# Optimization experiments

Hardware: AMD Instinct MI355X
Metric: run time of the kernel (lower is better)

The kernel has to match this reference:

```python
import jax, jax.numpy as jnp
import numpy as np

B, L, D, N = 2, 2048, 1024, 16
DT = 0.1  # liquid scaler integration step


def setup_inputs() -> dict:
    key = jax.random.key(0)
    ks = jax.random.split(key, 10)
    def w(k, shape, scale=0.02):
        return jax.random.normal(k, shape, jnp.float32) * scale
    log_min, log_max = float(np.log(0.001)), float(np.log(0.1))
    dt_bias = jax.random.uniform(ks[1], (D,), jnp.float32) * (log_max - log_min) + log_min
    return {
        "x": jax.random.normal(ks[0], (B, L, D), jnp.float32),
        "delta_W": w(ks[2], (D, D)), "delta_b": jnp.zeros((D,), jnp.float32),
        "B_W": w(ks[3], (N, D)), "B_b": jnp.zeros((N,), jnp.float32),
        "C_W": w(ks[4], (N, D)), "C_b": jnp.zeros((N,), jnp.float32),
        "A_log": jnp.zeros((D, N), jnp.float32),
        "dt_bias": dt_bias,
        "tau": jnp.ones((N,), jnp.float32),
        "Wi_W": w(ks[5], (N, D)), "Wi_b": jnp.zeros((N,), jnp.float32),
        "Wr_W": w(ks[6], (N, N)),
        "sel_W": w(ks[7], (D, N)), "sel_b": jnp.zeros((D,), jnp.float32),
        "h0": jnp.zeros((1, N), jnp.float32),
    }


def reference(x, delta_W, delta_b, B_W, B_b, C_W, C_b, A_log, dt_bias, tau,
              Wi_W, Wi_b, Wr_W, sel_W, sel_b, h0):
    Bsz, Ls, Dm = x.shape
    Ns = A_log.shape[1]

    # --- LiquidTimeConstantScaler ---
    gc = x.mean(axis=1)                                # [B, D]
    inp_sig = gc @ Wi_W.T + Wi_b                       # [B, N]
    cur = jnp.broadcast_to(h0, (Bsz, Ns))              # [B, N]
    rec = cur @ Wr_W.T                                 # [B, N]
    tau_c = jnp.clip(tau, 0.1, 10.0)
    dh_dt = (-cur + jnp.tanh(inp_sig + rec)) / tau_c[None, :]
    new_h = cur + DT * dh_dt                           # [B, N]
    sel = jax.nn.sigmoid(new_h @ sel_W.T + sel_b)      # [B, D]
    xs = x * sel[:, None, :]                           # [B, L, D]

    # --- selective SSM discretization ---
    delta = jax.nn.softplus(xs @ delta_W.T + delta_b + dt_bias)  # [B, L, D]
    Bm = xs @ B_W.T + B_b                              # [B, L, N]
    Cm = xs @ C_W.T + C_b                              # [B, L, N]
    A = -jnp.exp(A_log)                                # [D, N]
    A_d = jnp.exp(A[None, None] * delta[..., None])    # [B, L, D, N]
    factor = jnp.where(jnp.abs(A)[None, None] < 1e-6,
                       delta[..., None], (A_d - 1.0) / A[None, None])
    B_d = factor * Bm[:, :, None, :]                   # [B, L, D, N]

    # --- linear recurrence over time via scan ---
    def step(h, inputs):
        Ad_t, Bd_t, x_t, C_t = inputs                  # [B,D,N],[B,D,N],[B,D],[B,N]
        h = Ad_t * h + Bd_t * x_t[..., None]
        y = jnp.einsum('bdn,bn->bd', h, C_t)
        return h, y

    h_init = jnp.zeros((Bsz, Dm, Ns), x.dtype)
    _, ys = jax.lax.scan(step, h_init,
                         (A_d.transpose(1, 0, 2, 3), B_d.transpose(1, 0, 2, 3),
                          xs.transpose(1, 0, 2), Cm.transpose(1, 0, 2)))
    return ys.transpose(1, 0, 2)                        # [B, L, D]
```

## Files before the change

kernel.cpp:

```cpp
#include <hip/hip_runtime.h>
#include <hip/hip_bf16.h>
#include <math.h>

#define B_ 2
#define L_ 2048
#define D_ 1024
#define N_ 16
#define CCH 64
#define TCH 32
#define NCOLS 1056
#define NPAD  1088

typedef unsigned short u16;
typedef __attribute__((ext_vector_type(8))) short short8v;
typedef __attribute__((ext_vector_type(8))) unsigned short ushort8v;
typedef __attribute__((ext_vector_type(4))) float f32x4;

__device__ __forceinline__ float softplusf(float z) {
  return fmaxf(z, 0.f) + log1pf(__expf(-fabsf(z)));
}

__device__ __forceinline__ u16 bf16rne(float f) {
  union { float f; unsigned u; } c; c.f = f;
  unsigned u = c.u;
  u += 0x7fffu + ((u >> 16) & 1u);
  return (u16)(u >> 16);
}

__device__ __forceinline__ float bf16tof(u16 v) {
  union { unsigned u; float f; } c;
  c.u = (unsigned)v << 16;
  return c.f;
}

__device__ __forceinline__ void gl_lds16(const void* g, const u16* lds_base,
                                         int byte_off) {
  byte_off = __builtin_amdgcn_readfirstlane(byte_off);
  __builtin_amdgcn_global_load_lds(
      (const __attribute__((address_space(1))) void*)g,
      (__attribute__((address_space(3))) void*)((const char*)lds_base + byte_off),
      16, 0, 0);
}

__global__ __launch_bounds__(256) void k_gc_pack(const float* __restrict__ x,
    float* __restrict__ part1, u16* __restrict__ xb) {
  int blk = blockIdx.x;
  int b = blk >> 8, lc = blk & 255;
  int tid = threadIdx.x;
  int r0 = b * L_ + lc * 8;
  float4 s = {0.f, 0.f, 0.f, 0.f};
  #pragma unroll
  for (int q = 0; q < 8; ++q) {
    size_t off = (size_t)(r0 + q) * D_ + tid * 4;
    float4 v = *(const float4*)(x + off);
    s.x += v.x; s.y += v.y; s.z += v.z; s.w += v.w;
    ushort4 r;
    r.x = bf16rne(v.x); r.y = bf16rne(v.y);
    r.z = bf16rne(v.z); r.w = bf16rne(v.w);
    *(ushort4*)(xb + off) = r;
  }
  *(float4*)(part1 + (size_t)blk * D_ + tid * 4) = s;
}

__global__ __launch_bounds__(256) void k_gc_red(const float* __restrict__ part1,
                                                float* __restrict__ part2) {
  int gid = blockIdx.x * 256 + threadIdx.x;
  int d = gid & 1023;
  int jc = (gid >> 10) & 15;
  int b = gid >> 14;
  float s = 0.f;
  #pragma unroll
  for (int t = 0; t < 16; ++t)
    s += part1[(size_t)(b * 256 + jc * 16 + t) * D_ + d];
  part2[gid] = s;
}

__global__ __launch_bounds__(256) void k_newh_sel(const float* __restrict__ part2,
    const float* __restrict__ Wi_W, const float* __restrict__ Wi_b,
    const float* __restrict__ Wr_W, const float* __restrict__ tau,
    const float* __restrict__ h0, const float* __restrict__ sel_W,
    const float* __restrict__ sel_b, float* __restrict__ selp) {
  __shared__ float gcs[B_ * D_];
  __shared__ float nh[B_ * N_];
  int tid = threadIdx.x;
  for (int idx = tid; idx < B_ * D_; idx += 256) {
    int b = idx >> 10, d = idx & (D_ - 1);
    float s = 0.f;
    #pragma unroll
    for (int lc = 0; lc < 16; ++lc)
      s += part2[(size_t)((b << 4) | lc) * D_ + d];
    gcs[idx] = s * (1.f / L_);
  }
  __syncthreads();
  if (tid < B_ * N_) {
    int b = tid >> 4, n = tid & 15;
    float inp = Wi_b[n];
    const float* g = gcs + b * D_;
    const float* w = Wi_W + n * D_;
    for (int d = 0; d < D_; d += 4) {
      float4 gv = *(const float4*)(g + d);
      float4 wv = *(const float4*)(w + d);
      inp += gv.x * wv.x + gv.y * wv.y + gv.z * wv.z + gv.w * wv.w;
    }
    float rec = 0.f;
    for (int m = 0; m < N_; ++m) rec += h0[m] * Wr_W[n * N_ + m];
    float th = tanhf(inp + rec);
    float tc = fminf(fmaxf(tau[n], 0.1f), 10.f);
    float cur = h0[n];
    nh[tid] = cur + 0.1f * ((th - cur) / tc);
  }
  __syncthreads();
  for (int i = tid; i < B_ * D_; i += 256) {
    int b = i >> 10, d = i & (D_ - 1);
    const float* w = sel_W + d * N_;
    const float* h = nh + b * N_;
    float z = sel_b[d];
    #pragma unroll
    for (int n = 0; n < N_; n += 4) {
      float4 wv = *(const float4*)(w + n);
      z += h[n] * wv.x + h[n + 1] * wv.y + h[n + 2] * wv.z + h[n + 3] * wv.w;
    }
    selp[i] = 1.f / (1.f + __expf(-z));
  }
}

__global__ __launch_bounds__(256) void k_pack_w(const float* __restrict__ dW,
    const float* __restrict__ B_W, const float* __restrict__ C_W,
    const float* __restrict__ sel, u16* __restrict__ Wp) {
  int gid = blockIdx.x * 256 + threadIdx.x;
  int b = blockIdx.y;
  size_t e = (size_t)gid * 8;
  int nn = (int)(e >> 10);
  int k = (int)(e & 1023);
  ushort8v r;
  if (nn < NCOLS) {
    const float* src = (nn < 1024) ? dW + (size_t)nn * 1024
                     : (nn < 1040) ? B_W + (size_t)(nn - 1024) * 1024
                                   : C_W + (size_t)(nn - 1040) * 1024;
    float4 s0 = *(const float4*)(src + k);
    float4 s1 = *(const float4*)(src + k + 4);
    const float* sp = sel + b * D_ + k;
    float4 e0 = *(const float4*)sp;
    float4 e1 = *(const float4*)(sp + 4);
    r[0] = bf16rne(s0.x * e0.x); r[1] = bf16rne(s0.y * e0.y);
    r[2] = bf16rne(s0.z * e0.z); r[3] = bf16rne(s0.w * e0.w);
    r[4] = bf16rne(s1.x * e1.x); r[5] = bf16rne(s1.y * e1.y);
    r[6] = bf16rne(s1.z * e1.z); r[7] = bf16rne(s1.w * e1.w);
  } else {
    r = (ushort8v)0;
  }
  *(ushort8v*)(Wp + (size_t)b * (NPAD * 1024) + e) = r;
}

__global__ __launch_bounds__(256) void k_gemm(
    const u16* __restrict__ xb, const u16* __restrict__ Wp,
    const float* __restrict__ delta_b, const float* __restrict__ dt_bias,
    const float* __restrict__ B_b, const float* __restrict__ C_b,
    float* __restrict__ delta, float* __restrict__ Bm, float* __restrict__ Cm) {
  __shared__ __align__(16) u16 lds[4][4096];
  int m0 = blockIdx.x * 64;
  int n0 = blockIdx.y * 64;
  int batch = blockIdx.x >> 5;
  const u16* wb = Wp + (size_t)batch * (NPAD * 1024);
  int tid = threadIdx.x;
  int w = tid >> 6, l = tid & 63;
  int wr = w >> 1, wc = w & 1;
  int srow = l >> 3;
  int ssl = (l & 7) ^ srow;

  f32x4 acc[2][2];
  #pragma unroll
  for (int m = 0; m < 2; ++m)
    #pragma unroll
    for (int n = 0; n < 2; ++n)
      acc[m][n] = (f32x4){0.f, 0.f, 0.f, 0.f};

  #define STAGE(kb, buf)                                                       \
    {                                                                          \
      _Pragma("unroll")                                                        \
      for (int q = 0; q < 2; ++q) {                                            \
        int row = w * 16 + q * 8 + srow;                                       \
        gl_lds16(xb + (size_t)(m0 + row) * 1024 + (kb) * 64 + ssl * 8,         \
                 &lds[0][0], (buf) * 8192 + (w * 16 + q * 8) * 128);           \
        gl_lds16(wb + (size_t)(n0 + row) * 1024 + (kb) * 64 + ssl * 8,         \
                 &lds[0][0], 16384 + (buf) * 8192 + (w * 16 + q * 8) * 128);   \
      }                                                                        \
    }

  int lr = l & 15, lh = l >> 4;

  #define CSTEP(cur)                                                           \
    {                                                                          \
      _Pragma("unroll")                                                        \
      for (int ks = 0; ks < 2; ++ks) {                                         \
        short8v a[2], bq[2];                                                   \
        _Pragma("unroll")                                                      \
        for (int m = 0; m < 2; ++m) {                                          \
          int r = wr * 32 + m * 16 + lr;                                       \
          int ps = (ks * 4 + lh) ^ (r & 7);                                    \
          a[m] = *(const short8v*)((const char*)&lds[0][0] + (cur) * 8192 + r * 128 + ps * 16);\
        }                                                                      \
        _Pragma("unroll")                                                      \
        for (int n = 0; n < 2; ++n) {                                          \
          int r = wc * 32 + n * 16 + lr;                                       \
          int ps = (ks * 4 + lh) ^ (r & 7);                                    \
          bq[n] = *(const short8v*)((const char*)&lds[0][0] + 16384 + (cur) * 8192 + r * 128 + ps * 16);\
        }                                                                      \
        _Pragma("unroll")                                                      \
        for (int m = 0; m < 2; ++m)                                            \
          _Pragma("unroll")                                                    \
          for (int n = 0; n < 2; ++n)                                          \
            acc[m][n] = __builtin_amdgcn_mfma_f32_16x16x32_bf16(a[m], bq[n],   \
                                                                acc[m][n], 0, 0, 0);\
      }                                                                        \
    }

  STAGE(0, 0);
  STAGE(1, 1);
  #pragma unroll
  for (int kb = 0; kb < 15; ++kb) {
    int cur = kb & 1;
    asm volatile("s_waitcnt vmcnt(4)" ::: "memory");
    __builtin_amdgcn_s_barrier();
    CSTEP(cur);
    asm volatile("s_waitcnt lgkmcnt(0)" ::: "memory");
    __builtin_amdgcn_s_barrier();
    if (kb < 14) STAGE(kb + 2, cur);
  }
  asm volatile("s_waitcnt vmcnt(0)" ::: "memory");
  __builtin_amdgcn_s_barrier();
  CSTEP(1);
  #undef STAGE
  #undef CSTEP

  int ibase = m0 + wr * 32 + lh * 4;
  int jbase = n0 + wc * 32 + lr;
  #pragma unroll
  for (int m = 0; m < 2; ++m) {
    #pragma unroll
    for (int n = 0; n < 2; ++n) {
      int j = jbase + n * 16;
      #pragma unroll
      for (int r = 0; r < 2 * 2; ++r) {
        int i = ibase + m * 16 + r;
        float v = acc[m][n][r];
        if (j < 1024) {
          delta[(size_t)i * D_ + j] = softplusf(v + delta_b[j] + dt_bias[j]);
        } else if (j < 1040) {
          Bm[i * N_ + (j - 1024)] = v + B_b[j - 1024];
        } else if (j < NCOLS) {
          Cm[i * N_ + (j - 1040)] = v + C_b[j - 1040];
        }
      }
    }
  }
}

__global__ __launch_bounds__(256) void k_scan1(const u16* __restrict__ xb,
    const float* __restrict__ sel, const float* __restrict__ delta,
    const float* __restrict__ Bm, const float* __restrict__ A_log,
    float* __restrict__ prodA, float* __restrict__ hend) {
  int gid = blockIdx.x * 256 + threadIdx.x;
  int nq = gid & 3;
  int d = (gid >> 2) & (D_ - 1);
  int c = (gid >> 12) & (CCH - 1);
  int b = gid >> 18;
  float A[4], rA[4];
  unsigned smallm = 0;
  {
    float4 a0 = *(const float4*)(A_log + d * N_ + nq * 4);
    float av[4] = {a0.x, a0.y, a0.z, a0.w};
    #pragma unroll
    for (int n = 0; n < 4; ++n) {
      float a = -__expf(av[n]);
      A[n] = a; rA[n] = 1.f / a;
      if (fabsf(a) < 1e-6f) smallm |= (1u << n);
    }
  }
  float selv = sel[b * D_ + d];
  float h[4], p[4];
  #pragma unroll
  for (int n = 0; n < 4; ++n) { h[n] = 0.f; p[n] = 1.f; }
  int row0 = b * L_ + c * TCH;
  const u16* xp = xb + (size_t)row0 * D_ + d;
  const float* dp = delta + (size_t)row0 * D_ + d;
  const float4* bmp = (const float4*)(Bm + (size_t)row0 * N_) + nq;
  #pragma unroll 4
  for (int s = 0; s < TCH; ++s) {
    float dlt = dp[(size_t)s * D_];
    float xv = bf16tof(xp[(size_t)s * D_]) * selv;
    float4 q0 = bmp[s * 4];
    float bmv[4] = {q0.x, q0.y, q0.z, q0.w};
    #pragma unroll
    for (int n = 0; n < 4; ++n) {
      float Ad = __expf(A[n] * dlt);
      float f = ((smallm >> n) & 1u) ? dlt : (Ad - 1.f) * rA[n];
      h[n] = Ad * h[n] + (f * bmv[n]) * xv;
      p[n] *= Ad;
    }
  }
  size_t base = ((size_t)(gid >> 2)) * N_ + nq * 4;
  *(float4*)(prodA + base) = make_float4(p[0], p[1], p[2], p[3]);
  *(float4*)(hend + base)  = make_float4(h[0], h[1], h[2], h[3]);
}

__global__ __launch_bounds__(256) void k_scan2(const float* __restrict__ prodA,
    const float* __restrict__ hend, float* __restrict__ hin) {
  int gid = blockIdx.x * 256 + threadIdx.x;
  int b = gid >> 14;
  int rem = gid & 16383;
  size_t base = ((size_t)(b * CCH) << 14) + rem;
  float H = 0.f;
  #pragma unroll
  for (int g = 0; g < 4; ++g) {
    float pg[16], hg[16];
    #pragma unroll
    for (int t = 0; t < 16; ++t) {
      size_t idx = base + ((size_t)(g * 16 + t) << 14);
      pg[t] = prodA[idx];
      hg[t] = hend[idx];
    }
    #pragma unroll
    for (int t = 0; t < 16; ++t) {
      size_t idx = base + ((size_t)(g * 16 + t) << 14);
      hin[idx] = H;
      H = pg[t] * H + hg[t];
    }
  }
}

__global__ __launch_bounds__(256) void k_scan3(const u16* __restrict__ xb,
    const float* __restrict__ sel, const float* __restrict__ delta,
    const float* __restrict__ Bm, const float* __restrict__ Cm,
    const float* __restrict__ A_log, const float* __restrict__ hin,
    float* __restrict__ out) {
  int gid = blockIdx.x * 256 + threadIdx.x;
  int nq = gid & 3;
  int d = (gid >> 2) & (D_ - 1);
  int c = (gid >> 12) & (CCH - 1);
  int b = gid >> 18;
  float A[4], rA[4];
  unsigned smallm = 0;
  {
    float4 a0 = *(const float4*)(A_log + d * N_ + nq * 4);
    float av[4] = {a0.x, a0.y, a0.z, a0.w};
    #pragma unroll
    for (int n = 0; n < 4; ++n) {
      float a = -__expf(av[n]);
      A[n] = a; rA[n] = 1.f / a;
      if (fabsf(a) < 1e-6f) smallm |= (1u << n);
    }
  }
  float selv = sel[b * D_ + d];
  float h[4];
  {
    size_t base = ((size_t)(gid >> 2)) * N_ + nq * 4;
    float4 v0 = *(const float4*)(hin + base);
    h[0] = v0.x; h[1] = v0.y; h[2] = v0.z; h[3] = v0.w;
  }
  int row0 = b * L_ + c * TCH;
  const u16* xp = xb + (size_t)row0 * D_ + d;
  const float* dp = delta + (size_t)row0 * D_ + d;
  const float4* bmp = (const float4*)(Bm + (size_t)row0 * N_) + nq;
  const float4* cmp = (const float4*)(Cm + (size_t)row0 * N_) + nq;
  float* op = out + (size_t)row0 * D_ + d;
  #pragma unroll 4
  for (int s = 0; s < TCH; ++s) {
    float dlt = dp[(size_t)s * D_];
    float xv = bf16tof(xp[(size_t)s * D_]) * selv;
    float4 q0 = bmp[s * 4];
    float4 r0 = cmp[s * 4];
    float bmv[4] = {q0.x, q0.y, q0.z, q0.w};
    float cmv[4] = {r0.x, r0.y, r0.z, r0.w};
    float yp = 0.f;
    #pragma unroll
    for (int n = 0; n < 4; ++n) {
      float Ad = __expf(A[n] * dlt);
      float f = ((smallm >> n) & 1u) ? dlt : (Ad - 1.f) * rA[n];
      h[n] = Ad * h[n] + (f * bmv[n]) * xv;
      yp += h[n] * cmv[n];
    }
    float y = yp + __shfl_xor(yp, 1, 64);
    y += __shfl_xor(y, 2, 64);
    if (nq == 0) op[(size_t)s * D_] = y;
  }
}

extern "C" void kernel_launch(void* const* d_in, const int* in_sizes, int n_in,
                              void* d_out, int out_size, void* d_ws, size_t ws_size,
                              hipStream_t stream) {
  const float* x       = (const float*)d_in[0];
  const float* deltaW  = (const float*)d_in[1];
  const float* deltab  = (const float*)d_in[2];
  const float* B_W     = (const float*)d_in[3];
  const float* B_b     = (const float*)d_in[4];
  const float* C_W     = (const float*)d_in[5];
  const float* C_b     = (const float*)d_in[6];
  const float* A_log   = (const float*)d_in[7];
  const float* dt_bias = (const float*)d_in[8];
  const float* tau     = (const float*)d_in[9];
  const float* Wi_W    = (const float*)d_in[10];
  const float* Wi_b    = (const float*)d_in[11];
  const float* Wr_W    = (const float*)d_in[12];
  const float* sel_W   = (const float*)d_in[13];
  const float* sel_b   = (const float*)d_in[14];
  const float* h0      = (const float*)d_in[15];
  float* out = (float*)d_out;

  float* ws    = (float*)d_ws;
  float* delta = ws;
  float* selp  = delta + 4194304;
  float* Bm    = selp + 2048;
  float* Cm    = Bm + 65536;
  u16*   xb    = (u16*)(Cm + 65536);
  u16*   Wp    = xb + 4194304;
  float* hin   = (float*)(Wp + 2228224);
  float* part1 = hin;
  float* part2 = hin + 524288;
  float* prodA = out;
  float* hend  = out + 2097152;

  hipLaunchKernelGGL(k_gc_pack, dim3(512), dim3(256), 0, stream, x, part1, xb);
  hipLaunchKernelGGL(k_gc_red, dim3(128), dim3(256), 0, stream, part1, part2);
  hipLaunchKernelGGL(k_newh_sel, dim3(1), dim3(256), 0, stream,
                     part2, Wi_W, Wi_b, Wr_W, tau, h0, sel_W, sel_b, selp);
  hipLaunchKernelGGL(k_pack_w, dim3(544, 2), dim3(256), 0, stream,
                     deltaW, B_W, C_W, selp, Wp);
  hipLaunchKernelGGL(k_gemm, dim3(64, 17), dim3(256), 0, stream,
                     xb, Wp, deltab, dt_bias, B_b, C_b, delta, Bm, Cm);
  hipLaunchKernelGGL(k_scan1, dim3(2048), dim3(256), 0, stream,
                     xb, selp, delta, Bm, A_log, prodA, hend);
  hipLaunchKernelGGL(k_scan2, dim3(128), dim3(256), 0, stream,
                     prodA, hend, hin);
  hipLaunchKernelGGL(k_scan3, dim3(2048), dim3(256), 0, stream,
                     xb, selp, delta, Bm, Cm, A_log, hin, out);
}
```

Measured before the change: 130.0 us.

## Store delta as bf16 and replace chunk decay products with summed delta

The GEMM epilogue now writes softplus delta as bf16 rather than fp32, halving the delta traffic written there and read by both scan passes. Scan pass one no longer stores per-state decay products. It stores one per-channel sum of delta per chunk, and the carry pass rebuilds each chunk's decay as exp(A*sum). This removes the 16-wide prodA buffer traffic at the cost of an exp per chunk step and reduced delta precision, which could affect accuracy.

```diff
diff --git a/kernel.cpp b/kernel.cpp
--- a/kernel.cpp
+++ b/kernel.cpp
@@ -156,7 +156,7 @@
     const u16* __restrict__ xb, const u16* __restrict__ Wp,
     const float* __restrict__ delta_b, const float* __restrict__ dt_bias,
     const float* __restrict__ B_b, const float* __restrict__ C_b,
-    float* __restrict__ delta, float* __restrict__ Bm, float* __restrict__ Cm) {
+    u16* __restrict__ dlt, float* __restrict__ Bm, float* __restrict__ Cm) {
   __shared__ __align__(16) u16 lds[4][4096];
   int m0 = blockIdx.x * 64;
   int n0 = blockIdx.y * 64;
@@ -245,7 +245,7 @@
         int i = ibase + m * 16 + r;
         float v = acc[m][n][r];
         if (j < 1024) {
-          delta[(size_t)i * D_ + j] = softplusf(v + delta_b[j] + dt_bias[j]);
+          dlt[(size_t)i * D_ + j] = bf16rne(softplusf(v + delta_b[j] + dt_bias[j]));
         } else if (j < 1040) {
           Bm[i * N_ + (j - 1024)] = v + B_b[j - 1024];
         } else if (j < NCOLS) {
@@ -257,9 +257,9 @@
 }
 
 __global__ __launch_bounds__(256) void k_scan1(const u16* __restrict__ xb,
-    const float* __restrict__ sel, const float* __restrict__ delta,
+    const float* __restrict__ sel, const u16* __restrict__ dlt,
     const float* __restrict__ Bm, const float* __restrict__ A_log,
-    float* __restrict__ prodA, float* __restrict__ hend) {
+    float* __restrict__ sdelta, float* __restrict__ hend) {
   int gid = blockIdx.x * 256 + threadIdx.x;
   int nq = gid & 3;
   int d = (gid >> 2) & (D_ - 1);
@@ -278,59 +278,64 @@
     }
   }
   float selv = sel[b * D_ + d];
-  float h[4], p[4];
-  #pragma unroll
-  for (int n = 0; n < 4; ++n) { h[n] = 0.f; p[n] = 1.f; }
+  float h[4];
+  float sdl = 0.f;
+  #pragma unroll
+  for (int n = 0; n < 4; ++n) h[n] = 0.f;
   int row0 = b * L_ + c * TCH;
   const u16* xp = xb + (size_t)row0 * D_ + d;
-  const float* dp = delta + (size_t)row0 * D_ + d;
+  const u16* dp = dlt + (size_t)row0 * D_ + d;
   const float4* bmp = (const float4*)(Bm + (size_t)row0 * N_) + nq;
   #pragma unroll 4
   for (int s = 0; s < TCH; ++s) {
-    float dlt = dp[(size_t)s * D_];
+    float dltv = bf16tof(dp[(size_t)s * D_]);
     float xv = bf16tof(xp[(size_t)s * D_]) * selv;
+    sdl += dltv;
     float4 q0 = bmp[s * 4];
     float bmv[4] = {q0.x, q0.y, q0.z, q0.w};
     #pragma unroll
     for (int n = 0; n < 4; ++n) {
-      float Ad = __expf(A[n] * dlt);
-      float f = ((smallm >> n) & 1u) ? dlt : (Ad - 1.f) * rA[n];
+      float Ad = __expf(A[n] * dltv);
+      float f = ((smallm >> n) & 1u) ? dltv : (Ad - 1.f) * rA[n];
       h[n] = Ad * h[n] + (f * bmv[n]) * xv;
-      p[n] *= Ad;
     }
   }
   size_t base = ((size_t)(gid >> 2)) * N_ + nq * 4;
-  *(float4*)(prodA + base) = make_float4(p[0], p[1], p[2], p[3]);
-  *(float4*)(hend + base)  = make_float4(h[0], h[1], h[2], h[3]);
-}
-
-__global__ __launch_bounds__(256) void k_scan2(const float* __restrict__ prodA,
-    const float* __restrict__ hend, float* __restrict__ hin) {
+  *(float4*)(hend + base) = make_float4(h[0], h[1], h[2], h[3]);
+  if (nq == 0) sdelta[gid >> 2] = sdl;
+}
+
+__global__ __launch_bounds__(256) void k_scan2(const float* __restrict__ sdelta,
+    const float* __restrict__ hend, const float* __restrict__ A_log,
+    float* __restrict__ hin) {
   int gid = blockIdx.x * 256 + threadIdx.x;
   int b = gid >> 14;
   int rem = gid & 16383;
-  size_t base = ((size_t)(b * CCH) << 14) + rem;
+  int d = rem >> 4;
+  float a = -__expf(A_log[rem]);
+  size_t hbase = ((size_t)(b * CCH) << 14) + rem;
+  const float* sdp = sdelta + b * (CCH * D_) + d;
   float H = 0.f;
   #pragma unroll
-  for (int g = 0; g < 4; ++g) {
-    float pg[16], hg[16];
-    #pragma unroll
-    for (int t = 0; t < 16; ++t) {
-      size_t idx = base + ((size_t)(g * 16 + t) << 14);
-      pg[t] = prodA[idx];
-      hg[t] = hend[idx];
-    }
-    #pragma unroll
-    for (int t = 0; t < 16; ++t) {
-      size_t idx = base + ((size_t)(g * 16 + t) << 14);
-      hin[idx] = H;
-      H = pg[t] * H + hg[t];
+  for (int g = 0; g < 8; ++g) {
+    float sd[8], hg[8];
+    #pragma unroll
+    for (int t = 0; t < 8; ++t) {
+      int c = g * 8 + t;
+      sd[t] = sdp[c * D_];
+      hg[t] = hend[hbase + ((size_t)c << 14)];
+    }
+    #pragma unroll
+    for (int t = 0; t < 8; ++t) {
+      int c = g * 8 + t;
+      hin[hbase + ((size_t)c << 14)] = H;
+      H = __expf(a * sd[t]) * H + hg[t];
     }
   }
 }
 
 __global__ __launch_bounds__(256) void k_scan3(const u16* __restrict__ xb,
-    const float* __restrict__ sel, const float* __restrict__ delta,
+    const float* __restrict__ sel, const u16* __restrict__ dlt,
     const float* __restrict__ Bm, const float* __restrict__ Cm,
     const float* __restrict__ A_log, const float* __restrict__ hin,
     float* __restrict__ out) {
@@ -360,13 +365,13 @@
   }
   int row0 = b * L_ + c * TCH;
   const u16* xp = xb + (size_t)row0 * D_ + d;
-  const float* dp = delta + (size_t)row0 * D_ + d;
+  const u16* dp = dlt + (size_t)row0 * D_ + d;
   const float4* bmp = (const float4*)(Bm + (size_t)row0 * N_) + nq;
   const float4* cmp = (const float4*)(Cm + (size_t)row0 * N_) + nq;
   float* op = out + (size_t)row0 * D_ + d;
   #pragma unroll 4
   for (int s = 0; s < TCH; ++s) {
-    float dlt = dp[(size_t)s * D_];
+    float dltv = bf16tof(dp[(size_t)s * D_]);
     float xv = bf16tof(xp[(size_t)s * D_]) * selv;
     float4 q0 = bmp[s * 4];
     float4 r0 = cmp[s * 4];
@@ -375,8 +380,8 @@
     float yp = 0.f;
     #pragma unroll
     for (int n = 0; n < 4; ++n) {
-      float Ad = __expf(A[n] * dlt);
-      float f = ((smallm >> n) & 1u) ? dlt : (Ad - 1.f) * rA[n];
+      float Ad = __expf(A[n] * dltv);
+      float f = ((smallm >> n) & 1u) ? dltv : (Ad - 1.f) * rA[n];
       h[n] = Ad * h[n] + (f * bmv[n]) * xv;
       yp += h[n] * cmv[n];
     }
@@ -407,18 +412,17 @@
   const float* h0      = (const float*)d_in[15];
   float* out = (float*)d_out;
 
-  float* ws    = (float*)d_ws;
-  float* delta = ws;
-  float* selp  = delta + 4194304;
+  u16*   dlt   = (u16*)d_ws;
+  float* selp  = (float*)(dlt + 4194304);
   float* Bm    = selp + 2048;
   float* Cm    = Bm + 65536;
   u16*   xb    = (u16*)(Cm + 65536);
   u16*   Wp    = xb + 4194304;
-  float* hin   = (float*)(Wp + 2228224);
+  float* sdelta= (float*)(Wp + 2228224);
+  float* hin   = sdelta + 131072;
   float* part1 = hin;
   float* part2 = hin + 524288;
-  float* prodA = out;
-  float* hend  = out + 2097152;
+  float* hend  = out;
 
   hipLaunchKernelGGL(k_gc_pack, dim3(512), dim3(256), 0, stream, x, part1, xb);
   hipLaunchKernelGGL(k_gc_red, dim3(128), dim3(256), 0, stream, part1, part2);
@@ -427,11 +431,11 @@
   hipLaunchKernelGGL(k_pack_w, dim3(544, 2), dim3(256), 0, stream,
                      deltaW, B_W, C_W, selp, Wp);
   hipLaunchKernelGGL(k_gemm, dim3(64, 17), dim3(256), 0, stream,
-                     xb, Wp, deltab, dt_bias, B_b, C_b, delta, Bm, Cm);
+                     xb, Wp, deltab, dt_bias, B_b, C_b, dlt, Bm, Cm);
   hipLaunchKernelGGL(k_scan1, dim3(2048), dim3(256), 0, stream,
-                     xb, selp, delta, Bm, A_log, prodA, hend);
+                     xb, selp, dlt, Bm, A_log, sdelta, hend);
   hipLaunchKernelGGL(k_scan2, dim3(128), dim3(256), 0, stream,
-                     prodA, hend, hin);
+                     sdelta, hend, A_log, hin);
   hipLaunchKernelGGL(k_scan3, dim3(2048), dim3(256), 0, stream,
-                     xb, selp, delta, Bm, Cm, A_log, hin, out);
-}
+                     xb, selp, dlt, Bm, Cm, A_log, hin, out);
+}
```

After: 139.7 us. 1.07x slower.
